# Kernel optimization log

Hardware: AMD Instinct MI355X
Metric: run time of the kernel (lower is better)

## Reference

```python
import jax, jax.numpy as jnp
import numpy as np

K = 16
NS = [2048, 512, 128]

def _knn(q, r, k):
    # q: [B,M,3] query centers, r: [B,N,3] reference points -> (idx [B,M,k], sqdist [B,M,k])
    d2 = (jnp.sum(q * q, -1)[:, :, None] + jnp.sum(r * r, -1)[:, None, :]
          - 2.0 * jnp.einsum('bmd,bnd->bmn', q, r))
    neg, idx = jax.lax.top_k(-d2, k)
    return idx, jnp.maximum(-neg, 0.0)

def _gather(feat, idx):
    # feat [B,N,C], idx [B,M,k] -> [B,M,k,C]
    return jax.vmap(lambda f, i: f[i])(feat, idx)

def _down(x, pos, n, W1, b1, W2, b2):
    # PointNet++-style TransitionDown: sample n centers, kNN group, rel-pos concat, shared MLP, max-pool
    centers = pos[:, :n]
    idx, _ = _knn(centers, pos, K)
    rel = _gather(pos, idx) - centers[:, :, None, :]           # [B,n,K,3]
    feat = jnp.concatenate([rel, _gather(x, idx)], -1)          # [B,n,K,C+3]
    h = jax.nn.relu(feat @ W1 + b1) @ W2 + b2                   # last_act=False
    return jnp.max(h, axis=2), centers

def _up(xc, pc, prv_feat, prv_pos, W, b):
    # TransitionUp: 3-NN inverse-distance interpolation + skip concat + pointwise conv1d
    idx, d2 = _knn(prv_pos, pc, 3)
    w = 1.0 / (d2 + 1e-8)
    w = w / jnp.sum(w, -1, keepdims=True)
    interp = jnp.sum(_gather(xc, idx) * w[..., None], axis=2)   # [B,Nprv,Cc]
    cat = jnp.concatenate([interp, prv_feat], -1)
    return jax.nn.relu(cat @ W + b)

def setup_inputs() -> dict:
    key = jax.random.key(0)
    ks = jax.random.split(key, 16)
    p = lambda k, s: jax.random.normal(k, s, jnp.float32) * 0.02
    B, N = 4, 8192
    return {
        'x': jax.random.normal(ks[0], (B, N, 3), jnp.float32),
        'pos': jax.random.uniform(ks[1], (B, N, 3), jnp.float32),
        'd0_W1': p(ks[2], (6, 128)),   'd0_b1': jnp.zeros((128,), jnp.float32),
        'd0_W2': p(ks[3], (128, 128)), 'd0_b2': jnp.zeros((128,), jnp.float32),
        'd1_W1': p(ks[4], (131, 256)), 'd1_b1': jnp.zeros((256,), jnp.float32),
        'd1_W2': p(ks[5], (256, 256)), 'd1_b2': jnp.zeros((256,), jnp.float32),
        'd2_W1': p(ks[6], (259, 512)), 'd2_b1': jnp.zeros((512,), jnp.float32),
        'd2_W2': p(ks[7], (512, 512)), 'd2_b2': jnp.zeros((512,), jnp.float32),
        'u0_W': p(ks[8], (768, 256)),  'u0_b': jnp.zeros((256,), jnp.float32),
        'u1_W': p(ks[9], (384, 128)),  'u1_b': jnp.zeros((128,), jnp.float32),
        'u2_W': p(ks[10], (134, 128)), 'u2_b': jnp.zeros((128,), jnp.float32),
        'f_W1': p(ks[11], (128, 128)), 'f_b1': jnp.zeros((128,), jnp.float32),
        'f_W2': p(ks[12], (128, 128)), 'f_b2': jnp.zeros((128,), jnp.float32),
    }

def reference(x, pos, d0_W1, d0_b1, d0_W2, d0_b2, d1_W1, d1_b1, d1_W2, d1_b2,
              d2_W1, d2_b1, d2_W2, d2_b2, u0_W, u0_b, u1_W, u1_b, u2_W, u2_b,
              f_W1, f_b1, f_W2, f_b2):
    pos0, x0 = pos, x
    # encoder (transition-down) with cached (pos, x) per scale
    x1, pos1 = _down(x0, pos0, NS[0], d0_W1, d0_b1, d0_W2, d0_b2)
    x2, pos2 = _down(x1, pos1, NS[1], d1_W1, d1_b1, d1_W2, d1_b2)
    x3, pos3 = _down(x2, pos2, NS[2], d2_W1, d2_b1, d2_W2, d2_b2)
    # decoder (transition-up) consuming the cache in reverse; last level concats raw pos to skip feat
    up = _up(x3, pos3, x2, pos2, u0_W, u0_b)
    up = _up(up, pos2, x1, pos1, u1_W, u1_b)
    prv0 = jnp.concatenate([x0, pos0], -1)
    up = _up(up, pos1, prv0, pos0, u2_W, u2_b)
    # feat_map_layer_out: two pointwise conv1d layers, last_act=False
    out = jax.nn.relu(up @ f_W1 + f_b1) @ f_W2 + f_b2
    return (out, pos0)
```

## Files before the change

### kernel.cpp

```cpp
#include <hip/hip_runtime.h>

#define NFULL 8192
#define BATCH 4

typedef unsigned long long u64;
typedef unsigned int u32;
typedef __attribute__((ext_vector_type(8))) short bf8_t;
typedef __attribute__((ext_vector_type(4))) float f4_t;

__device__ __forceinline__ u32 fbias(float f) {
  u32 u = __float_as_uint(f);
  return (u & 0x80000000u) ? ~u : (u | 0x80000000u);
}
__device__ __forceinline__ float funbias(u32 b) {
  u32 u = (b & 0x80000000u) ? (b & 0x7fffffffu) : ~b;
  return __uint_as_float(u);
}
__device__ __forceinline__ short f2bf(float f) {
  u32 u = __float_as_uint(f);
  u32 r = u + 0x7FFFu + ((u >> 16) & 1u);
  return (short)(r >> 16);
}

__device__ __forceinline__ void pack_tile_rt(const float* __restrict__ W,
                                             short* __restrict__ outp,
                                             int KDIM, int N, int tile, int lane) {
  int NT = N >> 4;
  int kt = tile / NT, nt = tile - kt * NT;
  int n = nt * 16 + (lane & 15);
  int k0 = kt * 32 + (lane >> 4) * 8;
  bf8_t v;
#pragma unroll
  for (int j = 0; j < 8; ++j) {
    int k = k0 + j;
    v[j] = (k < KDIM) ? f2bf(W[(size_t)k * N + n]) : (short)0;
  }
  *(bf8_t*)(outp + ((size_t)tile * 64 + lane) * 8) = v;
}

__device__ void pack_dispatch(int blk, int lane,
    const float* d0W1, short* d0W1p, const float* d0W2, short* d0W2p,
    const float* d1W1, short* d1W1p, const float* d1W2, short* d1W2p,
    const float* d2W1, short* d2W1p, const float* d2W2, short* d2W2p,
    const float* u2W, short* u2Wp, const float* fW1, short* fW1p,
    const float* fW2, short* fW2p,
    const float* u0W, short* u0Wp, const float* u1W, short* u1Wp,
    const float* pos, float* posOut) {
  if      (blk < 8)    pack_tile_rt(d0W1, d0W1p, 6, 128, blk, lane);
  else if (blk < 40)   pack_tile_rt(d0W2, d0W2p, 128, 128, blk - 8, lane);
  else if (blk < 120)  pack_tile_rt(d1W1, d1W1p, 131, 256, blk - 40, lane);
  else if (blk < 248)  pack_tile_rt(d1W2, d1W2p, 256, 256, blk - 120, lane);
  else if (blk < 536)  pack_tile_rt(d2W1, d2W1p, 259, 512, blk - 248, lane);
  else if (blk < 1048) pack_tile_rt(d2W2, d2W2p, 512, 512, blk - 536, lane);
  else if (blk < 1088) pack_tile_rt(u2W, u2Wp, 134, 128, blk - 1048, lane);
  else if (blk < 1120) pack_tile_rt(fW1, fW1p, 128, 128, blk - 1088, lane);
  else if (blk < 1152) pack_tile_rt(fW2, fW2p, 128, 128, blk - 1120, lane);
  else if (blk < 1536) pack_tile_rt(u0W, u0Wp, 768, 256, blk - 1152, lane);
  else if (blk < 1632) pack_tile_rt(u1W, u1Wp, 384, 128, blk - 1536, lane);
  else {
    int base = (blk - 1632) * 256;
#pragma unroll
    for (int j = 0; j < 4; ++j) {
      int i = base + lane + j * 64;
      posOut[i] = pos[i];
    }
  }
}

__global__ __launch_bounds__(256) void pre_kernel(
    const float* __restrict__ pos, float4* __restrict__ sortedA,
    int* __restrict__ csA, float4* __restrict__ sortedB, int* __restrict__ csB,
    float4* __restrict__ sortedC, int* __restrict__ csC,
    const float* d0W1, short* d0W1p, const float* d0W2, short* d0W2p,
    const float* d1W1, short* d1W1p, const float* d1W2, short* d1W2p,
    const float* d2W1, short* d2W1p, const float* d2W2, short* d2W2p,
    const float* u2W, short* u2Wp, const float* fW1, short* fW1p,
    const float* fW2, short* fW2p,
    const float* u0W, short* u0Wp, const float* u1W, short* u1Wp,
    float* posOut) {
  __shared__ int cnt[4096];
  __shared__ int partial[256];
  int bx = blockIdx.x, t = threadIdx.x;
  if (bx >= 12) {
    int tt = (bx - 12) * 4 + (t >> 6);
    pack_dispatch(tt, t & 63,
        d0W1, d0W1p, d0W2, d0W2p, d1W1, d1W1p, d1W2, d1W2p,
        d2W1, d2W1p, d2W2, d2W2p, u2W, u2Wp, fW1, fW1p, fW2, fW2p,
        u0W, u0Wp, u1W, u1Wp, pos, posOut);
    return;
  }
  int which = bx >> 2, b = bx & 3;
  int NREF = (which == 0) ? 8192 : (which == 1) ? 2048 : 512;
  int GR = (which == 0) ? 16 : 8;
  int NC = GR * GR * GR;
  float4* sorted = ((which == 0) ? sortedA : (which == 1) ? sortedB : sortedC)
                   + (size_t)b * NREF;
  int* cs = ((which == 0) ? csA + b * 4097 : (which == 1) ? csB + b * 513
                                           : csC + b * 513);
  const float* pb = pos + (size_t)b * NFULL * 3;
  for (int c = t; c < NC; c += 256) cnt[c] = 0;
  __syncthreads();
  for (int p = t; p < NREF; p += 256) {
    float x = pb[p * 3 + 0], y = pb[p * 3 + 1], z = pb[p * 3 + 2];
    int cx = min(max((int)(x * GR), 0), GR - 1);
    int cy = min(max((int)(y * GR), 0), GR - 1);
    int cz = min(max((int)(z * GR), 0), GR - 1);
    atomicAdd(&cnt[(cz * GR + cy) * GR + cx], 1);
  }
  __syncthreads();
  int chunk = (NC + 255) / 256;
  int s = 0;
  for (int i = 0; i < chunk; ++i) {
    int c = t * chunk + i;
    if (c < NC) s += cnt[c];
  }
  partial[t] = s;
  __syncthreads();
  if (t == 0) {
    int run = 0;
    for (int i = 0; i < 256; ++i) { int v = partial[i]; partial[i] = run; run += v; }
  }
  __syncthreads();
  int run = partial[t];
  for (int i = 0; i < chunk; ++i) {
    int c = t * chunk + i;
    if (c < NC) { int v = cnt[c]; cnt[c] = run; run += v; }
  }
  __syncthreads();
  for (int c = t; c < NC; c += 256) cs[c] = cnt[c];
  if (t == 0) cs[NC] = NREF;
  __syncthreads();
  for (int p = t; p < NREF; p += 256) {
    float x = pb[p * 3 + 0], y = pb[p * 3 + 1], z = pb[p * 3 + 2];
    int cx = min(max((int)(x * GR), 0), GR - 1);
    int cy = min(max((int)(y * GR), 0), GR - 1);
    int cz = min(max((int)(z * GR), 0), GR - 1);
    int slot = atomicAdd(&cnt[(cz * GR + cy) * GR + cx], 1);
    sorted[slot] = make_float4(x, y, z, __uint_as_float((u32)p));
  }
}

__device__ __forceinline__ void group_insert_g32(u32 m32, u64 ck, int slot16,
                                                 u64& val, u64& tau) {
  if (m32) {
    while (m32) {
      int src = __ffs(m32) - 1;
      m32 &= m32 - 1;
      u64 c = __shfl((unsigned long long)ck, src, 32);
      u64 prev = __shfl_up((unsigned long long)val, 1, 16);
      if (slot16 == 0) prev = 0ull;
      val = (val <= c) ? val : ((prev <= c) ? c : prev);
    }
    tau = __shfl((unsigned long long)val, 15, 16);
  }
}

__device__ __forceinline__ void first_round_sort32(u64 ck, int gl,
                                                   u64& val, u64& tau) {
  u64 v = ck;
#pragma unroll
  for (int size = 2; size <= 32; size <<= 1) {
#pragma unroll
    for (int stride = size >> 1; stride > 0; stride >>= 1) {
      u64 other = __shfl_xor((unsigned long long)v, stride, 32);
      bool ddd = ((gl & size) == 0);
      bool takeMin = (((gl & stride) == 0) == ddd);
      u64 mn = (v <= other) ? v : other;
      u64 mx = (v <= other) ? other : v;
      v = takeMin ? mn : mx;
    }
  }
  val = __shfl((unsigned long long)v, gl & 15, 32);
  tau = __shfl((unsigned long long)val, 15, 16);
}

__device__ __forceinline__ void scan_range_g32(const float4* __restrict__ sb,
    int s, int e, float qx, float qy, float qz, float qq,
    int g32, int gl, int slot16, u64& val, u64& tau) {
  for (int t0 = s; t0 < e; t0 += 32) {
    int j = t0 + gl;
    u64 ck = ~0ull;
    if (j < e) {
      float4 P = sb[j];
      float rr = P.x * P.x + P.y * P.y + P.z * P.z;
      float d2 = qq + rr - 2.0f * (qx * P.x + qy * P.y + qz * P.z);
      ck = ((u64)fbias(d2) << 32) | (u32)__float_as_uint(P.w);
    }
    u64 full = __ballot(ck < tau);
    u32 m32 = (u32)(full >> (g32 * 32));
    group_insert_g32(m32, ck, slot16, val, tau);
  }
}
// ... 19 lines not shown
    int Y0 = max(iy - (R + 1), 0), Y1 = min(iy + (R + 1), GR - 1);
    int Z0 = max(iz - (R + 1), 0), Z1 = min(iz + (R + 1), GR - 1);
    int NY2 = Y1 - Y0 + 1;
    int nrow2 = (Z1 - Z0 + 1) * NY2;
    for (int rr2 = 0; rr2 < nrow2; ++rr2) {
      int zz = Z0 + rr2 / NY2, yy = Y0 + rr2 % NY2;
      int c0 = (zz * GR + yy) * GR;
      bool mid = (zz >= z0 && zz <= z1 && yy >= y0 && yy <= y1);
      int s1 = cs[c0 + X0];
      int e1 = mid ? cs[c0 + x0] : cs[c0 + X1 + 1];
      scan_range_g32(sb, s1, e1, qx, qy, qz, qq, g32, gl, slot16, val, tau);
      if (mid) {
        int s2 = cs[c0 + x1 + 1];
        int e2 = cs[c0 + X1 + 1];
        scan_range_g32(sb, s2, e2, qx, qy, qz, qq, g32, gl, slot16, val, tau);
      }
    }
    x0 = X0; x1 = X1; y0 = Y0; y1 = Y1; z0 = Z0; z1 = Z1;
    m = 1e30f;
    if (x0 > 0)      m = fminf(m, qx - x0 * h);
    if (x1 < GR - 1) m = fminf(m, (x1 + 1) * h - qx);
    if (y0 > 0)      m = fminf(m, qy - y0 * h);
    if (y1 < GR - 1) m = fminf(m, (y1 + 1) * h - qy);
    if (z0 > 0)      m = fminf(m, qz - z0 * h);
    if (z1 < GR - 1) m = fminf(m, (z1 + 1) * h - qz);
    bound = m * m;
    kth_d2 = funbias((u32)(tau >> 32));
    if (!(kth_d2 < bound)) {
      for (int t0 = 0; t0 < NREF; t0 += 32) {
        int j = t0 + gl;
        u64 ck = ~0ull;
        if (j < NREF) {
          float4 P = sb[j];
          int cx = min(max((int)(P.x * GR), 0), GR - 1);
          int cy = min(max((int)(P.y * GR), 0), GR - 1);
          int cz = min(max((int)(P.z * GR), 0), GR - 1);
          bool inbox = (cx >= x0 && cx <= x1 && cy >= y0 && cy <= y1 &&
                        cz >= z0 && cz <= z1);
          if (!inbox) {
            float rr = P.x * P.x + P.y * P.y + P.z * P.z;
            float d2 = qq + rr - 2.0f * (qx * P.x + qy * P.y + qz * P.z);
            ck = ((u64)fbias(d2) << 32) | (u32)__float_as_uint(P.w);
          }
        }
        u64 full = __ballot(ck < tau);
        u32 m32 = (u32)(full >> (g32 * 32));
        group_insert_g32(m32, ck, slot16, val, tau);
      }
    }
  }
}

template<int GR, int R, int NREF>
__device__ void knn_grid16_g32_dev(int vbx,
    const float* __restrict__ pos, const float4* __restrict__ sorted,
    const int* __restrict__ cellStart, int csStride, int Mq,
    int* __restrict__ oidx) {
  int b = blockIdx.y;
  int wv = threadIdx.x >> 6, lane = threadIdx.x & 63;
  int g32 = lane >> 5, gl = lane & 31;
  int q = vbx * 8 + wv * 2 + g32;
  const float* pb = pos + (size_t)b * NFULL * 3;
  const float4* sb = sorted + (size_t)b * NREF;
  const int* cs = cellStart + b * csStride;
  float qx = pb[q * 3 + 0], qy = pb[q * 3 + 1], qz = pb[q * 3 + 2];
  float qq = qx * qx + qy * qy + qz * qz;
  int ix = min(max((int)(qx * GR), 0), GR - 1);
  int iy = min(max((int)(qy * GR), 0), GR - 1);
  int iz = min(max((int)(qz * GR), 0), GR - 1);
  int x0 = max(ix - R, 0), x1 = min(ix + R, GR - 1);
  int y0 = max(iy - R, 0), y1 = min(iy + R, GR - 1);
  int z0 = max(iz - R, 0), z1 = min(iz + R, GR - 1);

  int ny = y1 - y0 + 1;
  int nrow = (z1 - z0 + 1) * ny;
  int s_i = 0, len_i = 0;
  if (gl < nrow) {
    int zz = z0 + gl / ny, yy = y0 + gl % ny;
    int c0 = (zz * GR + yy) * GR + x0;
    s_i = cs[c0];
    len_i = cs[c0 + (x1 - x0) + 1] - s_i;
  }
  int p_i = len_i;
#pragma unroll
  for (int st = 1; st < 32; st <<= 1) {
    int o = __shfl_up(p_i, st, 32);
    if (gl >= st) p_i += o;
  }
  int T = __shfl(p_i, 31, 32);
  p_i -= len_i;
  int d_i = s_i - p_i;
  if (gl >= nrow) p_i = 0x7fffffff;

  int slot16 = lane & 15;
  u64 val, tau;

  {
    int v = gl;
    int r = 0;
#pragma unroll
    for (int st = 16; st >= 1; st >>= 1) {
      int pc = __shfl(p_i, r + st, 32);
      if (v >= pc) r += st;
    }
    int addr = v + __shfl(d_i, r, 32);
    u64 ck = ~0ull;
    if (v < T) {
      float4 P = sb[addr];
      float rr = P.x * P.x + P.y * P.y + P.z * P.z;
      float d2 = qq + rr - 2.0f * (qx * P.x + qy * P.y + qz * P.z);
      ck = ((u64)fbias(d2) << 32) | (u32)__float_as_uint(P.w);
    }
    first_round_sort32(ck, gl, val, tau);
  }

  for (int v0 = 32; v0 < T; v0 += 32) {
    int v = v0 + gl;
    int r = 0;
#pragma unroll
    for (int st = 16; st >= 1; st >>= 1) {
      int pc = __shfl(p_i, r + st, 32);
      if (v >= pc) r += st;
    }
    int addr = v + __shfl(d_i, r, 32);
    u64 ck = ~0ull;
    if (v < T) {
      float4 P = sb[addr];
      float rr = P.x * P.x + P.y * P.y + P.z * P.z;
      float d2 = qq + rr - 2.0f * (qx * P.x + qy * P.y + qz * P.z);
      ck = ((u64)fbias(d2) << 32) | (u32)__float_as_uint(P.w);
    }
    u64 full = __ballot(ck < tau);
    u32 m32 = (u32)(full >> (g32 * 32));
    group_insert_g32(m32, ck, slot16, val, tau);
  }

  knn_tail16_g32<GR, R, NREF>(sb, cs, qx, qy, qz, qq,
      ix, iy, iz, x0, x1, y0, y1, z0, z1, g32, gl, slot16, val, tau);

  if (gl < 16) {
    size_t base = ((size_t)b * Mq + q) * 16;
    oidx[base + gl] = (int)(u32)val;
  }
}

__device__ void knn_brute16_g32_dev(int vbx,
    const float* __restrict__ pos, int Nref, int Mq, int* __restrict__ oidx) {
  int b = blockIdx.y;
  int wv = threadIdx.x >> 6, lane = threadIdx.x & 63;
  int g32 = lane >> 5, gl = lane & 31;
  int q = vbx * 8 + wv * 2 + g32;
  const float* pb = pos + (size_t)b * NFULL * 3;
  float qx = pb[q * 3 + 0], qy = pb[q * 3 + 1], qz = pb[q * 3 + 2];
  float qq = qx * qx + qy * qy + qz * qz;

  int slot16 = lane & 15;
  u64 val, tau;

  {
    int j = gl;
    float rx = pb[j * 3 + 0];
    float ry = pb[j * 3 + 1];
    float rz = pb[j * 3 + 2];
    float rr = rx * rx + ry * ry + rz * rz;
    float d2 = qq + rr - 2.0f * (qx * rx + qy * ry + qz * rz);
    u64 ck = ((u64)fbias(d2) << 32) | (u32)j;
    first_round_sort32(ck, gl, val, tau);
  }

  for (int t0 = 32; t0 < Nref; t0 += 32) {
    int j = t0 + gl;
    float rx = pb[j * 3 + 0];
    float ry = pb[j * 3 + 1];
    float rz = pb[j * 3 + 2];
    float rr = rx * rx + ry * ry + rz * rz;
    float d2 = qq + rr - 2.0f * (qx * rx + qy * ry + qz * rz);
    u64 ck = ((u64)fbias(d2) << 32) | (u32)j;
    u64 full = __ballot(ck < tau);
    u32 m32 = (u32)(full >> (g32 * 32));
    group_insert_g32(m32, ck, slot16, val, tau);
  }

  if (gl < 16) {
    size_t base = ((size_t)b * Mq + q) * 16;
    oidx[base + gl] = (int)(u32)val;
  }
}

__device__ __forceinline__ void lane_insert3(u64 ck, u64& v0, u64& v1, u64& v2) {
  u64 a = (v0 <= ck) ? v0 : ck;
  u64 bb = (v0 <= ck) ? ck : v0;
  v0 = a;
  u64 c = (v1 <= bb) ? v1 : bb;
  u64 d = (v1 <= bb) ? bb : v1;
  v1 = c;
  v2 = (v2 <= d) ? v2 : d;
}

__device__ __forceinline__ void merge3(u64 v0, u64 v1, u64 v2,
                                       u64& o0, u64& o1, u64& o2) {
  u64 h = v0;
// ... 49 lines not shown
    int X0 = max(ix - (R + 1), 0), X1 = min(ix + (R + 1), GR - 1);
    int Y0 = max(iy - (R + 1), 0), Y1 = min(iy + (R + 1), GR - 1);
    int Z0 = max(iz - (R + 1), 0), Z1 = min(iz + (R + 1), GR - 1);
    int NY2 = Y1 - Y0 + 1;
    int nrow2 = (Z1 - Z0 + 1) * NY2;
    for (int rr2 = 0; rr2 < nrow2; ++rr2) {
      int zz = Z0 + rr2 / NY2, yy = Y0 + rr2 % NY2;
      int c0 = (zz * GR + yy) * GR;
      bool mid = (zz >= z0 && zz <= z1 && yy >= y0 && yy <= y1);
      int s1 = cs[c0 + X0];
      int e1 = mid ? cs[c0 + x0] : cs[c0 + X1 + 1];
      scan_range3(sb, s1, e1, qx, qy, qz, qq, gl, v0, v1, v2);
      if (mid) {
        int s2 = cs[c0 + x1 + 1];
        int e2 = cs[c0 + X1 + 1];
        scan_range3(sb, s2, e2, qx, qy, qz, qq, gl, v0, v1, v2);
      }
    }
    x0 = X0; x1 = X1; y0 = Y0; y1 = Y1; z0 = Z0; z1 = Z1;
    m = 1e30f;
    if (x0 > 0)      m = fminf(m, qx - x0 * h);
    if (x1 < GR - 1) m = fminf(m, (x1 + 1) * h - qx);
    if (y0 > 0)      m = fminf(m, qy - y0 * h);
    if (y1 < GR - 1) m = fminf(m, (y1 + 1) * h - qy);
    if (z0 > 0)      m = fminf(m, qz - z0 * h);
    if (z1 < GR - 1) m = fminf(m, (z1 + 1) * h - qz);
    bound = m * m;
    merge3(v0, v1, v2, o0, o1, o2);
    kth_d2 = funbias((u32)(o2 >> 32));
    if (!(kth_d2 < bound)) {
      for (int t0 = 0; t0 < NREF; t0 += 16) {
        int j = t0 + gl;
        if (j < NREF) {
          float4 P = sb[j];
          int cx = min(max((int)(P.x * GR), 0), GR - 1);
          int cy = min(max((int)(P.y * GR), 0), GR - 1);
          int cz = min(max((int)(P.z * GR), 0), GR - 1);
          bool inbox = (cx >= x0 && cx <= x1 && cy >= y0 && cy <= y1 &&
                        cz >= z0 && cz <= z1);
          if (!inbox) {
            float rr = P.x * P.x + P.y * P.y + P.z * P.z;
            float d2 = qq + rr - 2.0f * (qx * P.x + qy * P.y + qz * P.z);
            u64 ck = ((u64)fbias(d2) << 32) | (u32)__float_as_uint(P.w);
            lane_insert3(ck, v0, v1, v2);
          }
        }
      }
      merge3(v0, v1, v2, o0, o1, o2);
    }
  }
}

template<int GR, int R, int NREF>
__device__ void knn_grid_flat3_dev(int vbx,
    const float* __restrict__ pos, const float4* __restrict__ sorted,
    const int* __restrict__ cellStart, int csStride, int Mq,
    int* __restrict__ oidx, float* __restrict__ od2) {
  int b = blockIdx.y;
  int wv = threadIdx.x >> 6, lane = threadIdx.x & 63;
  int g = lane >> 4, gl = lane & 15;
  int q = vbx * 16 + wv * 4 + g;
  const float* pb = pos + (size_t)b * NFULL * 3;
  const float4* sb = sorted + (size_t)b * NREF;
  const int* cs = cellStart + b * csStride;
  float qx = pb[q * 3 + 0], qy = pb[q * 3 + 1], qz = pb[q * 3 + 2];
  float qq = qx * qx + qy * qy + qz * qz;
  int ix = min(max((int)(qx * GR), 0), GR - 1);
  int iy = min(max((int)(qy * GR), 0), GR - 1);
  int iz = min(max((int)(qz * GR), 0), GR - 1);
  int x0 = max(ix - R, 0), x1 = min(ix + R, GR - 1);
  int y0 = max(iy - R, 0), y1 = min(iy + R, GR - 1);
  int z0 = max(iz - R, 0), z1 = min(iz + R, GR - 1);

  int ny = y1 - y0 + 1;
  int nrow = (z1 - z0 + 1) * ny;
  int s_i = 0, len_i = 0;
  if (gl < nrow) {
    int zz = z0 + gl / ny, yy = y0 + gl % ny;
    int c0 = (zz * GR + yy) * GR + x0;
    s_i = cs[c0];
    len_i = cs[c0 + (x1 - x0) + 1] - s_i;
  }
  int p_i = len_i;
#pragma unroll
  for (int st = 1; st < 16; st <<= 1) {
    int o = __shfl_up(p_i, st, 16);
    if (gl >= st) p_i += o;
  }
  int T = __shfl(p_i, 15, 16);
  p_i -= len_i;
  int d_i = s_i - p_i;
  if (gl >= nrow) p_i = 0x7fffffff;

  u64 v0 = ~0ull, v1 = ~0ull, v2 = ~0ull;

  for (int vb = 0; vb < T; vb += 16) {
    int v = vb + gl;
    int r = 0;
#pragma unroll
    for (int st = 8; st >= 1; st >>= 1) {
      int pc = __shfl(p_i, r + st, 16);
      if (v >= pc) r += st;
    }
    int addr = v + __shfl(d_i, r, 16);
    if (v < T) {
      float4 P = sb[addr];
      float rr = P.x * P.x + P.y * P.y + P.z * P.z;
      float d2 = qq + rr - 2.0f * (qx * P.x + qy * P.y + qz * P.z);
      u64 ck = ((u64)fbias(d2) << 32) | (u32)__float_as_uint(P.w);
      lane_insert3(ck, v0, v1, v2);
    }
  }

  u64 o0, o1, o2;
  knn_tail3<GR, R, NREF>(sb, cs, qx, qy, qz, qq,
      ix, iy, iz, x0, x1, y0, y1, z0, z1, gl, v0, v1, v2, o0, o1, o2);

  if (gl < 3) {
    u64 val = (gl == 0) ? o0 : ((gl == 1) ? o1 : o2);
    size_t base = ((size_t)b * Mq + q) * 3;
    oidx[base + gl] = (int)(u32)val;
    od2[base + gl] = fmaxf(funbias((u32)(val >> 32)), 0.0f);
  }
}

template<int GR, int R, int NREF>
__device__ void knn_grid_flat32_3_dev(int vbx,
    const float* __restrict__ pos, const float4* __restrict__ sorted,
    const int* __restrict__ cellStart, int csStride, int Mq,
    int* __restrict__ oidx, float* __restrict__ od2) {
  int b = blockIdx.y;
  int wv = threadIdx.x >> 6, lane = threadIdx.x & 63;
  int g = lane >> 4, gl = lane & 15;
  int q = vbx * 16 + wv * 4 + g;
  const float* pb = pos + (size_t)b * NFULL * 3;
  const float4* sb = sorted + (size_t)b * NREF;
  const int* cs = cellStart + b * csStride;
  float qx = pb[q * 3 + 0], qy = pb[q * 3 + 1], qz = pb[q * 3 + 2];
  float qq = qx * qx + qy * qy + qz * qz;
  int ix = min(max((int)(qx * GR), 0), GR - 1);
  int iy = min(max((int)(qy * GR), 0), GR - 1);
  int iz = min(max((int)(qz * GR), 0), GR - 1);
  int x0 = max(ix - R, 0), x1 = min(ix + R, GR - 1);
  int y0 = max(iy - R, 0), y1 = min(iy + R, GR - 1);
  int z0 = max(iz - R, 0), z1 = min(iz + R, GR - 1);

  int ny = y1 - y0 + 1;
  int nrow = (z1 - z0 + 1) * ny;
  int sLo = 0, lenLo = 0, sHi = 0, lenHi = 0;
  if (gl < nrow) {
    int zz = z0 + gl / ny, yy = y0 + gl % ny;
    int c0 = (zz * GR + yy) * GR + x0;
    sLo = cs[c0]; lenLo = cs[c0 + (x1 - x0) + 1] - sLo;
  }
  {
    int i2 = gl + 16;
    if (i2 < nrow) {
      int zz = z0 + i2 / ny, yy = y0 + i2 % ny;
      int c0 = (zz * GR + yy) * GR + x0;
      sHi = cs[c0]; lenHi = cs[c0 + (x1 - x0) + 1] - sHi;
    }
  }
  int pLo = lenLo, pHi = lenHi;
#pragma unroll
  for (int st = 1; st < 16; st <<= 1) {
    int o = __shfl_up(pLo, st, 16);
    if (gl >= st) pLo += o;
    int o2_ = __shfl_up(pHi, st, 16);
    if (gl >= st) pHi += o2_;
  }
  int tot16 = __shfl(pLo, 15, 16);
  pHi += tot16;
  int T = __shfl(pHi, 15, 16);
  pLo -= lenLo; pHi -= lenHi;
  int dLo = sLo - pLo, dHi = sHi - pHi;
  if (gl >= nrow) pLo = 0x7fffffff;
  if (gl + 16 >= nrow) pHi = 0x7fffffff;

  u64 v0 = ~0ull, v1 = ~0ull, v2 = ~0ull;

  for (int vb = 0; vb < T; vb += 16) {
    int v = vb + gl;
    int r = 0;
#pragma unroll
    for (int st = 16; st >= 1; st >>= 1) {
      int j = r + st;
      int pcL = __shfl(pLo, j & 15, 16);
      int pcH = __shfl(pHi, j & 15, 16);
      int pc = (j < 16) ? pcL : pcH;
      if (v >= pc) r = j;
    }
    int dL = __shfl(dLo, r & 15, 16);
    int dH = __shfl(dHi, r & 15, 16);
    int addr = v + ((r < 16) ? dL : dH);
    if (v < T) {
      float4 P = sb[addr];
      float rr = P.x * P.x + P.y * P.y + P.z * P.z;
      float d2 = qq + rr - 2.0f * (qx * P.x + qy * P.y + qz * P.z);
      u64 ck = ((u64)fbias(d2) << 32) | (u32)__float_as_uint(P.w);
      lane_insert3(ck, v0, v1, v2);
    }
  }

  u64 o0, o1, o2;
  knn_tail3<GR, R, NREF>(sb, cs, qx, qy, qz, qq,
      ix, iy, iz, x0, x1, y0, y1, z0, z1, gl, v0, v1, v2, o0, o1, o2);

  if (gl < 3) {
    u64 val = (gl == 0) ? o0 : ((gl == 1) ? o1 : o2);
    size_t base = ((size_t)b * Mq + q) * 3;
    oidx[base + gl] = (int)(u32)val;
    od2[base + gl] = fmaxf(funbias((u32)(val >> 32)), 0.0f);
  }
}

__device__ void knn_brute3_dev(int vbx,
    const float* __restrict__ pos, int Nref, int Mq,
    int* __restrict__ oidx, float* __restrict__ od2) {
  int b = blockIdx.y;
  int wv = threadIdx.x >> 6, lane = threadIdx.x & 63;
  int g = lane >> 4, gl = lane & 15;
  int q = vbx * 16 + wv * 4 + g;
  const float* pb = pos + (size_t)b * NFULL * 3;
  float qx = pb[q * 3 + 0], qy = pb[q * 3 + 1], qz = pb[q * 3 + 2];
  float qq = qx * qx + qy * qy + qz * qz;

  u64 v0 = ~0ull, v1 = ~0ull, v2 = ~0ull;
  for (int j = gl; j < Nref; j += 16) {
    float rx = pb[j * 3 + 0];
    float ry = pb[j * 3 + 1];
    float rz = pb[j * 3 + 2];
    float rr = rx * rx + ry * ry + rz * rz;
    float d2 = qq + rr - 2.0f * (qx * rx + qy * ry + qz * rz);
    u64 ck = ((u64)fbias(d2) << 32) | (u32)j;
    lane_insert3(ck, v0, v1, v2);
  }
  u64 o0, o1, o2;
  merge3(v0, v1, v2, o0, o1, o2);

  if (gl < 3) {
    u64 val = (gl == 0) ? o0 : ((gl == 1) ? o1 : o2);
    size_t base = ((size_t)b * Mq + q) * 3;
    oidx[base + gl] = (int)(u32)val;
    od2[base + gl] = fmaxf(funbias((u32)(val >> 32)), 0.0f);
  }
}

__global__ __launch_bounds__(256) void knn_all_kernel(
    const float* __restrict__ pos,
    const float4* __restrict__ sortedA, const int* __restrict__ csA,
    const float4* __restrict__ sortedB, const int* __restrict__ csB,
    const float4* __restrict__ sortedC, const int* __restrict__ csC,
    int* __restrict__ idx0, int* __restrict__ idx1, int* __restrict__ idx2,
    int* __restrict__ idxu0, float* __restrict__ d2u0,
    int* __restrict__ idxu1, float* __restrict__ d2u1,
    int* __restrict__ idxu2, float* __restrict__ d2u2) {
  int bx = blockIdx.x;
  if (bx < 16)
    knn_brute16_g32_dev(bx, pos, 512, 128, idx2);
  else if (bx < 80)
    knn_grid16_g32_dev<8, 2, 2048>(bx - 16, pos, sortedB, csB, 513, 512, idx1);
  else if (bx < 336)
    knn_grid16_g32_dev<16, 2, 8192>(bx - 80, pos, sortedA, csA, 4097, 2048, idx0);
  else if (bx < 464)
    knn_grid_flat32_3_dev<8, 2, 512>(bx - 336, pos, sortedC, csC, 513, 2048, idxu1, d2u1);
  else if (bx < 976)
    knn_grid_flat3_dev<8, 1, 2048>(bx - 464, pos, sortedB, csB, 513, 8192, idxu2, d2u2);
  else
    knn_brute3_dev(bx - 976, pos, 128, 512, idxu0, d2u0);
}

template<int FEAT, int CIN, int CHID, int FPAD, int QB, int WAVES>
__global__ __launch_bounds__(64 * WAVES) void down_mfma_kernel(
    const float* __restrict__ pos, const float* __restrict__ xin,
    const int* __restrict__ idx,
    const short* __restrict__ W1p, const float* __restrict__ b1,
    const short* __restrict__ W2p, const float* __restrict__ b2,
    float* __restrict__ out, int n, int nprev) {
  const int KT1 = FPAD / 32, NT1 = CHID / 16;
  const int KT2 = CHID / 32, NT2 = CHID / 16;
  __shared__ short sFeat[QB][16][FPAD + 8];
  __shared__ short sH1[QB][16][CHID + 8];
  __shared__ int sIdx[QB][16];
  __shared__ float sCtr[QB][3];
  int b = blockIdx.y, q0 = blockIdx.x * QB;
  int t = threadIdx.x;
  int lane = t & 63, wv = t >> 6;
  const float* pb = pos + (size_t)b * NFULL * 3;
  const float* xb = xin + (size_t)b * nprev * CIN;
  if (t < QB * 16)
    sIdx[t >> 4][t & 15] = idx[((size_t)b * n + q0 + (t >> 4)) * 16 + (t & 15)];
  if (t < QB * 3) sCtr[t / 3][t % 3] = pb[(q0 + t / 3) * 3 + (t % 3)];
  __syncthreads();
  for (int e = t; e < QB * 16 * FPAD; e += 64 * WAVES) {
    int k = e / FPAD, c = e - k * FPAD;
    int qq = k >> 4, kk = k & 15;
    float v = 0.f;
    if (c < 3) v = pb[sIdx[qq][kk] * 3 + c] - sCtr[qq][c];
    else if (c < FEAT) v = xb[(size_t)sIdx[qq][kk] * CIN + (c - 3)];
    sFeat[qq][kk][c] = f2bf(v);
  }
  __syncthreads();

  int col = lane & 15, quad = lane >> 4;
  const bf8_t* W1t = (const bf8_t*)W1p;
  for (int nt = 2 * wv; nt < NT1; nt += 2 * WAVES) {
    f4_t acc[QB][2];
    float bb0 = b1[nt * 16 + col], bb1 = b1[nt * 16 + 16 + col];
#pragma unroll
    for (int q = 0; q < QB; ++q) {
      acc[q][0] = {bb0, bb0, bb0, bb0};
      acc[q][1] = {bb1, bb1, bb1, bb1};
    }
#pragma unroll
    for (int kt = 0; kt < KT1; ++kt) {
      bf8_t bf0 = W1t[(kt * NT1 + nt) * 64 + lane];
      bf8_t bf1 = W1t[(kt * NT1 + nt + 1) * 64 + lane];
#pragma unroll
      for (int q = 0; q < QB; ++q) {
        bf8_t a = *(const bf8_t*)&sFeat[q][col][kt * 32 + quad * 8];
        acc[q][0] = __builtin_amdgcn_mfma_f32_16x16x32_bf16(a, bf0, acc[q][0], 0, 0, 0);
        acc[q][1] = __builtin_amdgcn_mfma_f32_16x16x32_bf16(a, bf1, acc[q][1], 0, 0, 0);
      }
    }
#pragma unroll
    for (int q = 0; q < QB; ++q)
#pragma unroll
      for (int r = 0; r < 4; ++r) {
        sH1[q][quad * 4 + r][nt * 16 + col] = f2bf(fmaxf(acc[q][0][r], 0.f));
        sH1[q][quad * 4 + r][nt * 16 + 16 + col] = f2bf(fmaxf(acc[q][1][r], 0.f));
      }
  }
  __syncthreads();

  const bf8_t* W2t = (const bf8_t*)W2p;
  for (int nt = 2 * wv; nt < NT2; nt += 2 * WAVES) {
    f4_t acc[QB][2];
    float bb0 = b2[nt * 16 + col], bb1 = b2[nt * 16 + 16 + col];
#pragma unroll
    for (int q = 0; q < QB; ++q) {
      acc[q][0] = {bb0, bb0, bb0, bb0};
      acc[q][1] = {bb1, bb1, bb1, bb1};
    }
#pragma unroll
    for (int kt = 0; kt < KT2; ++kt) {
      bf8_t bf0 = W2t[(kt * NT2 + nt) * 64 + lane];
      bf8_t bf1 = W2t[(kt * NT2 + nt + 1) * 64 + lane];
#pragma unroll
      for (int q = 0; q < QB; ++q) {
        bf8_t a = *(const bf8_t*)&sH1[q][col][kt * 32 + quad * 8];
        acc[q][0] = __builtin_amdgcn_mfma_f32_16x16x32_bf16(a, bf0, acc[q][0], 0, 0, 0);
        acc[q][1] = __builtin_amdgcn_mfma_f32_16x16x32_bf16(a, bf1, acc[q][1], 0, 0, 0);
      }
    }
#pragma unroll
    for (int q = 0; q < QB; ++q) {
      float m0 = fmaxf(fmaxf(acc[q][0][0], acc[q][0][1]), fmaxf(acc[q][0][2], acc[q][0][3]));
      float m1 = fmaxf(fmaxf(acc[q][1][0], acc[q][1][1]), fmaxf(acc[q][1][2], acc[q][1][3]));
      m0 = fmaxf(m0, __shfl_xor(m0, 16, 64));
      m0 = fmaxf(m0, __shfl_xor(m0, 32, 64));
      m1 = fmaxf(m1, __shfl_xor(m1, 16, 64));
      m1 = fmaxf(m1, __shfl_xor(m1, 32, 64));
      if (lane < 16) {
        float* ob = out + ((size_t)b * n + q0 + q) * CHID;
        ob[nt * 16 + lane] = m0;
        ob[nt * 16 + 16 + lane] = m1;
      }
    }
  }
}

template<int CIN, int CPRV, int COUT, int WPB>
__global__ __launch_bounds__(64 * WPB) void up_mfma_kernel(
    const float* __restrict__ xc, int ncoarse,
    const int* __restrict__ idx3, const float* __restrict__ d23,
    const float* __restrict__ prv, const short* __restrict__ Wp,
    const float* __restrict__ bvec, float* __restrict__ out, int m) {
  const int CTOT = CIN + CPRV;
  const int KT = CTOT / 32, NT = COUT / 16;
  __shared__ short sA[16][CTOT + 8];
  __shared__ float sWt[16][3];
  __shared__ int   sIt[16][3];
  int b = blockIdx.y, q0 = blockIdx.x * 16, t = threadIdx.x;
  int lane = t & 63, wv = t >> 6;
  if (t < 16) {
    size_t base = ((size_t)b * m + q0 + t) * 3;
    float d0 = d23[base + 0], d1 = d23[base + 1], d2v = d23[base + 2];
    float w0 = 1.f / (d0 + 1e-8f), w1 = 1.f / (d1 + 1e-8f), w2 = 1.f / (d2v + 1e-8f);
    float s = w0 + w1 + w2;
    sWt[t][0] = w0 / s; sWt[t][1] = w1 / s; sWt[t][2] = w2 / s;
    sIt[t][0] = idx3[base + 0]; sIt[t][1] = idx3[base + 1]; sIt[t][2] = idx3[base + 2];
  }
  __syncthreads();
  const float* xb = xc + (size_t)b * ncoarse * CIN;
  const float* pvb = prv + ((size_t)b * m + q0) * CPRV;
  for (int e = t; e < 16 * CIN; e += 64 * WPB) {
    int p = e / CIN, c = e % CIN;
    float v = sWt[p][0] * xb[(size_t)sIt[p][0] * CIN + c]
            + sWt[p][1] * xb[(size_t)sIt[p][1] * CIN + c]
            + sWt[p][2] * xb[(size_t)sIt[p][2] * CIN + c];
    sA[p][c] = f2bf(v);
  }
  for (int e = t; e < 16 * CPRV; e += 64 * WPB) {
    int p = e / CPRV, c = e % CPRV;
    sA[p][CIN + c] = f2bf(pvb[(size_t)p * CPRV + c]);
  }
  __syncthreads();
  int col = lane & 15, quad = lane >> 4;
  const bf8_t* Wt = (const bf8_t*)Wp;
  float* ob = out + ((size_t)b * m + q0) * COUT;
  for (int nt = 2 * wv; nt < NT; nt += 2 * WPB) {
    float bb0 = bvec[nt * 16 + col], bb1 = bvec[nt * 16 + 16 + col];
    f4_t acc0 = {bb0, bb0, bb0, bb0}, acc1 = {bb1, bb1, bb1, bb1};
#pragma unroll
    for (int kt = 0; kt < KT; ++kt) {
      bf8_t a = *(const bf8_t*)&sA[col][kt * 32 + quad * 8];
      bf8_t bf0 = Wt[(kt * NT + nt) * 64 + lane];
      bf8_t bf1 = Wt[(kt * NT + nt + 1) * 64 + lane];
      acc0 = __builtin_amdgcn_mfma_f32_16x16x32_bf16(a, bf0, acc0, 0, 0, 0);
      acc1 = __builtin_amdgcn_mfma_f32_16x16x32_bf16(a, bf1, acc1, 0, 0, 0);
    }
#pragma unroll
// ... 128 lines not shown
  const float* d1b1 = (const float*)d_in[7];
  const float* d1W2 = (const float*)d_in[8];
  const float* d1b2 = (const float*)d_in[9];
  const float* d2W1 = (const float*)d_in[10];
  const float* d2b1 = (const float*)d_in[11];
  const float* d2W2 = (const float*)d_in[12];
  const float* d2b2 = (const float*)d_in[13];
  const float* u0W  = (const float*)d_in[14];
  const float* u0b  = (const float*)d_in[15];
  const float* u1W  = (const float*)d_in[16];
  const float* u1b  = (const float*)d_in[17];
  const float* u2W  = (const float*)d_in[18];
  const float* u2b  = (const float*)d_in[19];
  const float* fW1  = (const float*)d_in[20];
  const float* fb1  = (const float*)d_in[21];
  const float* fW2  = (const float*)d_in[22];
  const float* fb2  = (const float*)d_in[23];

  char* ws = (char*)d_ws;
  float* x1    = (float*)(ws + 0);
  float* x2    = (float*)(ws + 4194304);
  float* x3    = (float*)(ws + 6291456);
  float* up0o  = (float*)(ws + 7340032);
  float* up1o  = (float*)(ws + 9437184);
  int*   idx0  = (int*)  (ws + 13631488);
  int*   idx1  = (int*)  (ws + 14155776);
  int*   idx2  = (int*)  (ws + 14286848);
  float4* sortedC = (float4*)(ws + 14319616);
  int*    csC     = (int*)   (ws + 14352384);
  int*   idxu0 = (int*)  (ws + 14843904);
  float* d2u0  = (float*)(ws + 14868480);
  int*   idxu1 = (int*)  (ws + 14893056);
  float* d2u1  = (float*)(ws + 14991360);
  int*   idxu2 = (int*)  (ws + 15089664);
  float* d2u2  = (float*)(ws + 15482880);
  short* d1W1p = (short*)(ws + 15876096);
  short* d1W2p = (short*)(ws + 15958016);
  short* d2W1p = (short*)(ws + 16089088);
  short* d2W2p = (short*)(ws + 16384000);
  short* d0W1p = (short*)(ws + 16908288);
  short* d0W2p = (short*)(ws + 16916480);
  float4* sortedA = (float4*)(ws + 16949248);
  int*    csA     = (int*)   (ws + 17473536);
  float4* sortedB = (float4*)(ws + 17539136);
  int*    csB     = (int*)   (ws + 17670208);
  short* u2Wp  = (short*)(ws + 17697920);
  short* fW1p  = (short*)(ws + 17738880);
  short* fW2p  = (short*)(ws + 17771648);

  float* out = (float*)d_out;
  short* u0Wp = (short*)out;
  short* u1Wp = (short*)(out + 98304);

  pre_kernel<<<dim3(516), 256, 0, stream>>>(
      pos, sortedA, csA, sortedB, csB, sortedC, csC,
      d0W1, d0W1p, d0W2, d0W2p, d1W1, d1W1p, d1W2, d1W2p,
      d2W1, d2W1p, d2W2, d2W2p, u2W, u2Wp, fW1, fW1p, fW2, fW2p,
      u0W, u0Wp, u1W, u1Wp,
      out + (size_t)BATCH * NFULL * 128);

  knn_all_kernel<<<dim3(1008, BATCH), 256, 0, stream>>>(
      pos, sortedA, csA, sortedB, csB, sortedC, csC,
      idx0, idx1, idx2,
      idxu0, d2u0, idxu1, d2u1, idxu2, d2u2);

  down_mfma_kernel<6, 3, 128, 32, 4, 4><<<dim3(512, BATCH), 256, 0, stream>>>(
      pos, x, idx0, d0W1p, d0b1, d0W2p, d0b2, x1, 2048, 8192);
  down_mfma_kernel<131, 128, 256, 160, 4, 8><<<dim3(128, BATCH), 512, 0, stream>>>(
      pos, x1, idx1, d1W1p, d1b1, d1W2p, d1b2, x2, 512, 2048);
  down_mfma_kernel<259, 256, 512, 288, 2, 8><<<dim3(64, BATCH), 512, 0, stream>>>(
      pos, x2, idx2, d2W1p, d2b1, d2W2p, d2b2, x3, 128, 512);

  up_mfma_kernel<512, 256, 256, 4><<<dim3(32, BATCH), 256, 0, stream>>>(
      x3, 128, idxu0, d2u0, x2, u0Wp, u0b, up0o, 512);
  up_mfma_kernel<256, 128, 128, 2><<<dim3(128, BATCH), 128, 0, stream>>>(
      up0o, 512, idxu1, d2u1, x1, u1Wp, u1b, up1o, 2048);
  up2f_mfma_kernel<<<dim3(512, BATCH), 128, 0, stream>>>(
      up1o, idxu2, d2u2, x, pos, u2Wp, u2b, fW1p, fb1, fW2p, fb2, out);
}
```

Before: 290.1 us.

## Redistribute kNN work across pre, knn16 and down0 kernels for overlap

The brute-force kNN searches that need no spatial grid (idx2 and idxu0) move into the preprocessing kernel as extra blocks. The 3-NN grid searches for the up layers are fused into the first down-MLP kernel as extra blocks. The remaining kNN kernel now handles only the two 16-NN grid searches. The aim is to fill idle compute units by running independent work in the same launches and to shorten the serial kNN kernel. The fused kernels now mix heterogeneous blocks, which can raise register and LDS pressure and make load balance uneven.

```diff
diff --git a/kernel.cpp b/kernel.cpp
--- a/kernel.cpp
+++ b/kernel.cpp
@@ -20,124 +20,6 @@
   u32 u = __float_as_uint(f);
   u32 r = u + 0x7FFFu + ((u >> 16) & 1u);
   return (short)(r >> 16);
-}
-
-__device__ __forceinline__ void pack_tile_rt(const float* __restrict__ W,
-                                             short* __restrict__ outp,
-                                             int KDIM, int N, int tile, int lane) {
-  int NT = N >> 4;
-  int kt = tile / NT, nt = tile - kt * NT;
-  int n = nt * 16 + (lane & 15);
-  int k0 = kt * 32 + (lane >> 4) * 8;
-  bf8_t v;
-#pragma unroll
-  for (int j = 0; j < 8; ++j) {
-    int k = k0 + j;
-    v[j] = (k < KDIM) ? f2bf(W[(size_t)k * N + n]) : (short)0;
-  }
-  *(bf8_t*)(outp + ((size_t)tile * 64 + lane) * 8) = v;
-}
-
-__device__ void pack_dispatch(int blk, int lane,
-    const float* d0W1, short* d0W1p, const float* d0W2, short* d0W2p,
-    const float* d1W1, short* d1W1p, const float* d1W2, short* d1W2p,
-    const float* d2W1, short* d2W1p, const float* d2W2, short* d2W2p,
-    const float* u2W, short* u2Wp, const float* fW1, short* fW1p,
-    const float* fW2, short* fW2p,
-    const float* u0W, short* u0Wp, const float* u1W, short* u1Wp,
-    const float* pos, float* posOut) {
-  if      (blk < 8)    pack_tile_rt(d0W1, d0W1p, 6, 128, blk, lane);
-  else if (blk < 40)   pack_tile_rt(d0W2, d0W2p, 128, 128, blk - 8, lane);
-  else if (blk < 120)  pack_tile_rt(d1W1, d1W1p, 131, 256, blk - 40, lane);
-  else if (blk < 248)  pack_tile_rt(d1W2, d1W2p, 256, 256, blk - 120, lane);
-  else if (blk < 536)  pack_tile_rt(d2W1, d2W1p, 259, 512, blk - 248, lane);
-  else if (blk < 1048) pack_tile_rt(d2W2, d2W2p, 512, 512, blk - 536, lane);
-  else if (blk < 1088) pack_tile_rt(u2W, u2Wp, 134, 128, blk - 1048, lane);
-  else if (blk < 1120) pack_tile_rt(fW1, fW1p, 128, 128, blk - 1088, lane);
-  else if (blk < 1152) pack_tile_rt(fW2, fW2p, 128, 128, blk - 1120, lane);
-  else if (blk < 1536) pack_tile_rt(u0W, u0Wp, 768, 256, blk - 1152, lane);
-  else if (blk < 1632) pack_tile_rt(u1W, u1Wp, 384, 128, blk - 1536, lane);
-  else {
-    int base = (blk - 1632) * 256;
-#pragma unroll
-    for (int j = 0; j < 4; ++j) {
-      int i = base + lane + j * 64;
-      posOut[i] = pos[i];
-    }
-  }
-}
-
-__global__ __launch_bounds__(256) void pre_kernel(
-    const float* __restrict__ pos, float4* __restrict__ sortedA,
-    int* __restrict__ csA, float4* __restrict__ sortedB, int* __restrict__ csB,
-    float4* __restrict__ sortedC, int* __restrict__ csC,
-    const float* d0W1, short* d0W1p, const float* d0W2, short* d0W2p,
-    const float* d1W1, short* d1W1p, const float* d1W2, short* d1W2p,
-    const float* d2W1, short* d2W1p, const float* d2W2, short* d2W2p,
-    const float* u2W, short* u2Wp, const float* fW1, short* fW1p,
-    const float* fW2, short* fW2p,
-    const float* u0W, short* u0Wp, const float* u1W, short* u1Wp,
-    float* posOut) {
-  __shared__ int cnt[4096];
-  __shared__ int partial[256];
-  int bx = blockIdx.x, t = threadIdx.x;
-  if (bx >= 12) {
-    int tt = (bx - 12) * 4 + (t >> 6);
-    pack_dispatch(tt, t & 63,
-        d0W1, d0W1p, d0W2, d0W2p, d1W1, d1W1p, d1W2, d1W2p,
-        d2W1, d2W1p, d2W2, d2W2p, u2W, u2Wp, fW1, fW1p, fW2, fW2p,
-        u0W, u0Wp, u1W, u1Wp, pos, posOut);
-    return;
-  }
-  int which = bx >> 2, b = bx & 3;
-  int NREF = (which == 0) ? 8192 : (which == 1) ? 2048 : 512;
-  int GR = (which == 0) ? 16 : 8;
-  int NC = GR * GR * GR;
-  float4* sorted = ((which == 0) ? sortedA : (which == 1) ? sortedB : sortedC)
-                   + (size_t)b * NREF;
-  int* cs = ((which == 0) ? csA + b * 4097 : (which == 1) ? csB + b * 513
-                                           : csC + b * 513);
-  const float* pb = pos + (size_t)b * NFULL * 3;
-  for (int c = t; c < NC; c += 256) cnt[c] = 0;
-  __syncthreads();
-  for (int p = t; p < NREF; p += 256) {
-    float x = pb[p * 3 + 0], y = pb[p * 3 + 1], z = pb[p * 3 + 2];
-    int cx = min(max((int)(x * GR), 0), GR - 1);
-    int cy = min(max((int)(y * GR), 0), GR - 1);
-    int cz = min(max((int)(z * GR), 0), GR - 1);
-    atomicAdd(&cnt[(cz * GR + cy) * GR + cx], 1);
-  }
-  __syncthreads();
-  int chunk = (NC + 255) / 256;
-  int s = 0;
-  for (int i = 0; i < chunk; ++i) {
-    int c = t * chunk + i;
-    if (c < NC) s += cnt[c];
-  }
-  partial[t] = s;
-  __syncthreads();
-  if (t == 0) {
-    int run = 0;
-    for (int i = 0; i < 256; ++i) { int v = partial[i]; partial[i] = run; run += v; }
-  }
-  __syncthreads();
-  int run = partial[t];
-  for (int i = 0; i < chunk; ++i) {
-    int c = t * chunk + i;
-    if (c < NC) { int v = cnt[c]; cnt[c] = run; run += v; }
-  }
-  __syncthreads();
-  for (int c = t; c < NC; c += 256) cs[c] = cnt[c];
-  if (t == 0) cs[NC] = NREF;
-  __syncthreads();
-  for (int p = t; p < NREF; p += 256) {
-    float x = pb[p * 3 + 0], y = pb[p * 3 + 1], z = pb[p * 3 + 2];
-    int cx = min(max((int)(x * GR), 0), GR - 1);
-    int cy = min(max((int)(y * GR), 0), GR - 1);
-    int cz = min(max((int)(z * GR), 0), GR - 1);
-    int slot = atomicAdd(&cnt[(cz * GR + cy) * GR + cx], 1);
-    sorted[slot] = make_float4(x, y, z, __uint_as_float((u32)p));
-  }
 }
 
 __device__ __forceinline__ void group_insert_g32(u32 m32, u64 ck, int slot16,
@@ -263,11 +145,10 @@
 }
 
 template<int GR, int R, int NREF>
-__device__ void knn_grid16_g32_dev(int vbx,
+__device__ void knn_grid16_g32_dev(int vbx, int b,
     const float* __restrict__ pos, const float4* __restrict__ sorted,
     const int* __restrict__ cellStart, int csStride, int Mq,
     int* __restrict__ oidx) {
-  int b = blockIdx.y;
   int wv = threadIdx.x >> 6, lane = threadIdx.x & 63;
   int g32 = lane >> 5, gl = lane & 31;
   int q = vbx * 8 + wv * 2 + g32;
@@ -355,9 +236,8 @@
   }
 }
 
-__device__ void knn_brute16_g32_dev(int vbx,
+__device__ void knn_brute16_g32_dev(int vbx, int b,
     const float* __restrict__ pos, int Nref, int Mq, int* __restrict__ oidx) {
-  int b = blockIdx.y;
   int wv = threadIdx.x >> 6, lane = threadIdx.x & 63;
   int g32 = lane >> 5, gl = lane & 31;
   int q = vbx * 8 + wv * 2 + g32;
@@ -513,11 +393,10 @@
 }
 
 template<int GR, int R, int NREF>
-__device__ void knn_grid_flat3_dev(int vbx,
+__device__ void knn_grid_flat3_dev(int vbx, int b,
     const float* __restrict__ pos, const float4* __restrict__ sorted,
     const int* __restrict__ cellStart, int csStride, int Mq,
     int* __restrict__ oidx, float* __restrict__ od2) {
-  int b = blockIdx.y;
   int wv = threadIdx.x >> 6, lane = threadIdx.x & 63;
   int g = lane >> 4, gl = lane & 15;
   int q = vbx * 16 + wv * 4 + g;
@@ -586,11 +465,10 @@
 }
 
 template<int GR, int R, int NREF>
-__device__ void knn_grid_flat32_3_dev(int vbx,
+__device__ void knn_grid_flat32_3_dev(int vbx, int b,
     const float* __restrict__ pos, const float4* __restrict__ sorted,
     const int* __restrict__ cellStart, int csStride, int Mq,
     int* __restrict__ oidx, float* __restrict__ od2) {
-  int b = blockIdx.y;
   int wv = threadIdx.x >> 6, lane = threadIdx.x & 63;
   int g = lane >> 4, gl = lane & 15;
   int q = vbx * 16 + wv * 4 + g;
@@ -675,10 +553,9 @@
   }
 }
 
-__device__ void knn_brute3_dev(int vbx,
+__device__ void knn_brute3_dev(int vbx, int b,
     const float* __restrict__ pos, int Nref, int Mq,
     int* __restrict__ oidx, float* __restrict__ od2) {
-  int b = blockIdx.y;
   int wv = threadIdx.x >> 6, lane = threadIdx.x & 63;
   int g = lane >> 4, gl = lane & 15;
   int q = vbx * 16 + wv * 4 + g;
@@ -707,32 +584,149 @@
   }
 }
 
-__global__ __launch_bounds__(256) void knn_all_kernel(
+__device__ __forceinline__ void pack_tile_rt(const float* __restrict__ W,
+                                             short* __restrict__ outp,
+                                             int KDIM, int N, int tile, int lane) {
+  int NT = N >> 4;
+  int kt = tile / NT, nt = tile - kt * NT;
+  int n = nt * 16 + (lane & 15);
+  int k0 = kt * 32 + (lane >> 4) * 8;
+  bf8_t v;
+#pragma unroll
+  for (int j = 0; j < 8; ++j) {
+    int k = k0 + j;
+    v[j] = (k < KDIM) ? f2bf(W[(size_t)k * N + n]) : (short)0;
+  }
+  *(bf8_t*)(outp + ((size_t)tile * 64 + lane) * 8) = v;
+}
+
+__device__ void pack_dispatch(int blk, int lane,
+    const float* d0W1, short* d0W1p, const float* d0W2, short* d0W2p,
+    const float* d1W1, short* d1W1p, const float* d1W2, short* d1W2p,
+    const float* d2W1, short* d2W1p, const float* d2W2, short* d2W2p,
+    const float* u2W, short* u2Wp, const float* fW1, short* fW1p,
+    const float* fW2, short* fW2p,
+    const float* u0W, short* u0Wp, const float* u1W, short* u1Wp,
+    const float* pos, float* posOut) {
+  if      (blk < 8)    pack_tile_rt(d0W1, d0W1p, 6, 128, blk, lane);
+  else if (blk < 40)   pack_tile_rt(d0W2, d0W2p, 128, 128, blk - 8, lane);
+  else if (blk < 120)  pack_tile_rt(d1W1, d1W1p, 131, 256, blk - 40, lane);
+  else if (blk < 248)  pack_tile_rt(d1W2, d1W2p, 256, 256, blk - 120, lane);
+  else if (blk < 536)  pack_tile_rt(d2W1, d2W1p, 259, 512, blk - 248, lane);
+  else if (blk < 1048) pack_tile_rt(d2W2, d2W2p, 512, 512, blk - 536, lane);
+  else if (blk < 1088) pack_tile_rt(u2W, u2Wp, 134, 128, blk - 1048, lane);
+  else if (blk < 1120) pack_tile_rt(fW1, fW1p, 128, 128, blk - 1088, lane);
+  else if (blk < 1152) pack_tile_rt(fW2, fW2p, 128, 128, blk - 1120, lane);
+  else if (blk < 1536) pack_tile_rt(u0W, u0Wp, 768, 256, blk - 1152, lane);
+  else if (blk < 1632) pack_tile_rt(u1W, u1Wp, 384, 128, blk - 1536, lane);
+  else {
+    int base = (blk - 1632) * 256;
+#pragma unroll
+    for (int j = 0; j < 4; ++j) {
+      int i = base + lane + j * 64;
+      posOut[i] = pos[i];
+    }
+  }
+}
+
+__global__ __launch_bounds__(256) void pre_kernel(
+    const float* __restrict__ pos, float4* __restrict__ sortedA,
+    int* __restrict__ csA, float4* __restrict__ sortedB, int* __restrict__ csB,
+    float4* __restrict__ sortedC, int* __restrict__ csC,
+    const float* d0W1, short* d0W1p, const float* d0W2, short* d0W2p,
+    const float* d1W1, short* d1W1p, const float* d1W2, short* d1W2p,
+    const float* d2W1, short* d2W1p, const float* d2W2, short* d2W2p,
+    const float* u2W, short* u2Wp, const float* fW1, short* fW1p,
+    const float* fW2, short* fW2p,
+    const float* u0W, short* u0Wp, const float* u1W, short* u1Wp,
+    float* posOut,
+    int* __restrict__ idx2, int* __restrict__ idxu0, float* __restrict__ d2u0) {
+  __shared__ int cnt[4096];
+  __shared__ int partial[256];
+  int bx = blockIdx.x, t = threadIdx.x;
+  if (bx >= 580) {
+    int i = bx - 580;
+    knn_brute3_dev(i & 31, i >> 5, pos, 128, 512, idxu0, d2u0);
+    return;
+  }
+  if (bx >= 516) {
+    int i = bx - 516;
+    knn_brute16_g32_dev(i & 15, i >> 4, pos, 512, 128, idx2);
+    return;
+  }
+  if (bx >= 12) {
+    int tt = (bx - 12) * 4 + (t >> 6);
+    pack_dispatch(tt, t & 63,
+        d0W1, d0W1p, d0W2, d0W2p, d1W1, d1W1p, d1W2, d1W2p,
+        d2W1, d2W1p, d2W2, d2W2p, u2W, u2Wp, fW1, fW1p, fW2, fW2p,
+        u0W, u0Wp, u1W, u1Wp, pos, posOut);
+    return;
+  }
+  int which = bx >> 2, b = bx & 3;
+  int NREF = (which == 0) ? 8192 : (which == 1) ? 2048 : 512;
+  int GR = (which == 0) ? 16 : 8;
+  int NC = GR * GR * GR;
+  float4* sorted = ((which == 0) ? sortedA : (which == 1) ? sortedB : sortedC)
+                   + (size_t)b * NREF;
+  int* cs = ((which == 0) ? csA + b * 4097 : (which == 1) ? csB + b * 513
+                                           : csC + b * 513);
+  const float* pb = pos + (size_t)b * NFULL * 3;
+  for (int c = t; c < NC; c += 256) cnt[c] = 0;
+  __syncthreads();
+  for (int p = t; p < NREF; p += 256) {
+    float x = pb[p * 3 + 0], y = pb[p * 3 + 1], z = pb[p * 3 + 2];
+    int cx = min(max((int)(x * GR), 0), GR - 1);
+    int cy = min(max((int)(y * GR), 0), GR - 1);
+    int cz = min(max((int)(z * GR), 0), GR - 1);
+    atomicAdd(&cnt[(cz * GR + cy) * GR + cx], 1);
+  }
+  __syncthreads();
+  int chunk = (NC + 255) / 256;
+  int s = 0;
+  for (int i = 0; i < chunk; ++i) {
+    int c = t * chunk + i;
+    if (c < NC) s += cnt[c];
+  }
+  partial[t] = s;
+  __syncthreads();
+  if (t == 0) {
+    int run = 0;
+    for (int i = 0; i < 256; ++i) { int v = partial[i]; partial[i] = run; run += v; }
+  }
+  __syncthreads();
+  int run = partial[t];
+  for (int i = 0; i < chunk; ++i) {
+    int c = t * chunk + i;
+    if (c < NC) { int v = cnt[c]; cnt[c] = run; run += v; }
+  }
+  __syncthreads();
+  for (int c = t; c < NC; c += 256) cs[c] = cnt[c];
+  if (t == 0) cs[NC] = NREF;
+  __syncthreads();
+  for (int p = t; p < NREF; p += 256) {
+    float x = pb[p * 3 + 0], y = pb[p * 3 + 1], z = pb[p * 3 + 2];
+    int cx = min(max((int)(x * GR), 0), GR - 1);
+    int cy = min(max((int)(y * GR), 0), GR - 1);
+    int cz = min(max((int)(z * GR), 0), GR - 1);
+    int slot = atomicAdd(&cnt[(cz * GR + cy) * GR + cx], 1);
+    sorted[slot] = make_float4(x, y, z, __uint_as_float((u32)p));
+  }
+}
+
+__global__ __launch_bounds__(256) void knn16_kernel(
     const float* __restrict__ pos,
     const float4* __restrict__ sortedA, const int* __restrict__ csA,
     const float4* __restrict__ sortedB, const int* __restrict__ csB,
-    const float4* __restrict__ sortedC, const int* __restrict__ csC,
-    int* __restrict__ idx0, int* __restrict__ idx1, int* __restrict__ idx2,
-    int* __restrict__ idxu0, float* __restrict__ d2u0,
-    int* __restrict__ idxu1, float* __restrict__ d2u1,
-    int* __restrict__ idxu2, float* __restrict__ d2u2) {
-  int bx = blockIdx.x;
-  if (bx < 16)
-    knn_brute16_g32_dev(bx, pos, 512, 128, idx2);
-  else if (bx < 80)
-    knn_grid16_g32_dev<8, 2, 2048>(bx - 16, pos, sortedB, csB, 513, 512, idx1);
-  else if (bx < 336)
-    knn_grid16_g32_dev<16, 2, 8192>(bx - 80, pos, sortedA, csA, 4097, 2048, idx0);
-  else if (bx < 464)
-    knn_grid_flat32_3_dev<8, 2, 512>(bx - 336, pos, sortedC, csC, 513, 2048, idxu1, d2u1);
-  else if (bx < 976)
-    knn_grid_flat3_dev<8, 1, 2048>(bx - 464, pos, sortedB, csB, 513, 8192, idxu2, d2u2);
+    int* __restrict__ idx0, int* __restrict__ idx1) {
+  int bx = blockIdx.x, b = blockIdx.y;
+  if (bx < 64)
+    knn_grid16_g32_dev<8, 2, 2048>(bx, b, pos, sortedB, csB, 513, 512, idx1);
   else
-    knn_brute3_dev(bx - 976, pos, 128, 512, idxu0, d2u0);
+    knn_grid16_g32_dev<16, 2, 8192>(bx - 64, b, pos, sortedA, csA, 4097, 2048, idx0);
 }
 
 template<int FEAT, int CIN, int CHID, int FPAD, int QB, int WAVES>
-__global__ __launch_bounds__(64 * WAVES) void down_mfma_kernel(
+__device__ void down_mfma_body(int bxx, int b,
     const float* __restrict__ pos, const float* __restrict__ xin,
     const int* __restrict__ idx,
     const short* __restrict__ W1p, const float* __restrict__ b1,
@@ -744,7 +738,7 @@
   __shared__ short sH1[QB][16][CHID + 8];
   __shared__ int sIdx[QB][16];
   __shared__ float sCtr[QB][3];
-  int b = blockIdx.y, q0 = blockIdx.x * QB;
+  int q0 = bxx * QB;
   int t = threadIdx.x;
   int lane = t & 63, wv = t >> 6;
   const float* pb = pos + (size_t)b * NFULL * 3;
@@ -829,6 +823,37 @@
       }
     }
   }
+}
+
+template<int FEAT, int CIN, int CHID, int FPAD, int QB, int WAVES>
+__global__ __launch_bounds__(64 * WAVES) void down_mfma_kernel(
+    const float* __restrict__ pos, const float* __restrict__ xin,
+    const int* __restrict__ idx,
+    const short* __restrict__ W1p, const float* __restrict__ b1,
+    const short* __restrict__ W2p, const float* __restrict__ b2,
+    float* __restrict__ out, int n, int nprev) {
+  down_mfma_body<FEAT, CIN, CHID, FPAD, QB, WAVES>(blockIdx.x, blockIdx.y,
+      pos, xin, idx, W1p, b1, W2p, b2, out, n, nprev);
+}
+
+__global__ __launch_bounds__(256) void down0_knn3_kernel(
+    const float* __restrict__ pos, const float* __restrict__ xin,
+    const int* __restrict__ idx,
+    const short* __restrict__ W1p, const float* __restrict__ b1,
+    const short* __restrict__ W2p, const float* __restrict__ b2,
+    float* __restrict__ out,
+    const float4* __restrict__ sortedB, const int* __restrict__ csB,
+    const float4* __restrict__ sortedC, const int* __restrict__ csC,
+    int* __restrict__ idxu1, float* __restrict__ d2u1,
+    int* __restrict__ idxu2, float* __restrict__ d2u2) {
+  int bx = blockIdx.x, b = blockIdx.y;
+  if (bx < 512)
+    down_mfma_body<6, 3, 128, 32, 4, 4>(bx, b, pos, xin, idx,
+        W1p, b1, W2p, b2, out, 2048, 8192);
+  else if (bx < 1024)
+    knn_grid_flat3_dev<8, 1, 2048>(bx - 512, b, pos, sortedB, csB, 513, 8192, idxu2, d2u2);
+  else
+    knn_grid_flat32_3_dev<8, 2, 512>(bx - 1024, b, pos, sortedC, csC, 513, 2048, idxu1, d2u1);
 }
 
 template<int CIN, int CPRV, int COUT, int WPB>
@@ -1063,20 +1088,21 @@
   short* u0Wp = (short*)out;
   short* u1Wp = (short*)(out + 98304);
 
-  pre_kernel<<<dim3(516), 256, 0, stream>>>(
+  pre_kernel<<<dim3(708), 256, 0, stream>>>(
       pos, sortedA, csA, sortedB, csB, sortedC, csC,
       d0W1, d0W1p, d0W2, d0W2p, d1W1, d1W1p, d1W2, d1W2p,
       d2W1, d2W1p, d2W2, d2W2p, u2W, u2Wp, fW1, fW1p, fW2, fW2p,
       u0W, u0Wp, u1W, u1Wp,
-      out + (size_t)BATCH * NFULL * 128);
-
-  knn_all_kernel<<<dim3(1008, BATCH), 256, 0, stream>>>(
-      pos, sortedA, csA, sortedB, csB, sortedC, csC,
-      idx0, idx1, idx2,
-      idxu0, d2u0, idxu1, d2u1, idxu2, d2u2);
-
-  down_mfma_kernel<6, 3, 128, 32, 4, 4><<<dim3(512, BATCH), 256, 0, stream>>>(
-      pos, x, idx0, d0W1p, d0b1, d0W2p, d0b2, x1, 2048, 8192);
+      out + (size_t)BATCH * NFULL * 128,
+      idx2, idxu0, d2u0);
+
+  knn16_kernel<<<dim3(320, BATCH), 256, 0, stream>>>(
+      pos, sortedA, csA, sortedB, csB, idx0, idx1);
+
+  down0_knn3_kernel<<<dim3(1152, BATCH), 256, 0, stream>>>(
+      pos, x, idx0, d0W1p, d0b1, d0W2p, d0b2, x1,
+      sortedB, csB, sortedC, csC, idxu1, d2u1, idxu2, d2u2);
+
   down_mfma_kernel<131, 128, 256, 160, 4, 8><<<dim3(128, BATCH), 512, 0, stream>>>(
       pos, x1, idx1, d1W1p, d1b1, d1W2p, d1b2, x2, 512, 2048);
   down_mfma_kernel<259, 256, 512, 288, 2, 8><<<dim3(64, BATCH), 512, 0, stream>>>(
```

Result: no change. 293.5 us (+1.2%).
